# Kernel optimization log

Hardware: AMD Instinct MI355X
Metric: run time of the kernel (lower is better)

Reference implementation:

```python
import jax, jax.numpy as jnp
import numpy as np

HEAD_DIM = 64
WINDOW = 32  # conv_kernel_size


def setup_inputs() -> dict:
    key = jax.random.key(0)
    k0, k1, k2, k3, k4 = jax.random.split(key, 5)
    B, S, H, D = 2, 2048, 8, HEAD_DIM
    return {
        "q": jax.random.normal(k0, (B, S, H * D), dtype=jnp.float32),
        "k": jax.random.normal(k1, (B, S, H * D), dtype=jnp.float32),
        "v": jax.random.normal(k2, (B, S, H * D), dtype=jnp.float32),
        "a": jax.random.normal(k3, (B, S, H), dtype=jnp.float32),
        "b": jax.random.normal(k4, (B, S, H), dtype=jnp.float32),
    }


def reference(q, k, v, a, b):
    B, S, _ = q.shape
    D = HEAD_DIM
    H = k.shape[-1] // D
    W = WINDOW
    scale = 1.0 / (D ** 0.5)

    qh = q.reshape(B, S, H, D)
    kh = k.reshape(B, S, H, D)
    vh = v.reshape(B, S, H, D)

    # window positions j = i - (W-1) + r, r in [0, W); mask j < 0 (torch slices them away)
    idx = jnp.arange(S)[:, None] - (W - 1) + jnp.arange(W)[None, :]  # [S, W]
    valid = (idx >= 0).astype(q.dtype)                               # [S, W]
    idxc = jnp.clip(idx, 0, S - 1)

    k_win = kh[:, idxc]   # [B, S, W, H, D]
    v_win = vh[:, idxc]   # [B, S, W, H, D]
    a_win = a[:, idxc]    # [B, S, W, H]

    scores = jnp.einsum('bshd,bswhd->bswh', qh, k_win) * scale       # [B, S, W, H]
    gates = jax.nn.sigmoid(a_win * b[:, :, None, :])                 # sigmoid(a_j * b_i)
    w = scores * gates * valid[None, :, :, None]

    out = jnp.einsum('bswh,bswhd->bshd', w, v_win)                   # [B, S, H, D]
    return out.reshape(B, S, H * D)
```

## Files before the change

kernel.cpp:

```cpp
#include <hip/hip_runtime.h>
#include <hip/hip_bf16.h>

#define S_LEN 2048
#define H_NUM 8
#define D_DIM 64
#define W_WIN 32

typedef short bf16x8 __attribute__((ext_vector_type(8)));
typedef float f32x4  __attribute__((ext_vector_type(4)));

__device__ __forceinline__ int kswz(int row, int b) {
    return (row << 7) + (b ^ ((row & 7) << 4));
}
__device__ __forceinline__ short f2bf(float x) {
    __hip_bfloat16 h = __float2bfloat16(x);
    return *reinterpret_cast<short*>(&h);
}
__device__ __forceinline__ bf16x8 pack8(float4 a, float4 b) {
    bf16x8 r;
    r[0] = f2bf(a.x); r[1] = f2bf(a.y); r[2] = f2bf(a.z); r[3] = f2bf(a.w);
    r[4] = f2bf(b.x); r[5] = f2bf(b.y); r[6] = f2bf(b.z); r[7] = f2bf(b.w);
    return r;
}
__device__ __forceinline__ int sclamp(int s) {
    return s < 0 ? 0 : (s > S_LEN - 1 ? S_LEN - 1 : s);
}

__global__ __launch_bounds__(64) void swa_gated_direct(
    const float* __restrict__ q, const float* __restrict__ k,
    const float* __restrict__ v, const float* __restrict__ a,
    const float* __restrict__ bgate, float* __restrict__ out)
{
    __shared__ __align__(16) unsigned short w_s[16 * 64];
    char* wb = (char*)w_s;

    const int l  = threadIdx.x;
    const int lr = l & 15;
    const int lk = l >> 4;

    const int bid  = blockIdx.x;
    const int orig = ((bid & 7) << 8) | (bid >> 3);
    const int tile = orig & 127;
    const int h    = (orig >> 7) & 7;
    const int bb   = orig >> 10;
    const int q0   = tile * 16;
    const size_t HD = (size_t)H_NUM * D_DIM;

    const float* qrow = q + ((size_t)(bb * S_LEN + q0 + lr)) * HD + (size_t)h * D_DIM + 8 * lk;
    bf16x8 aq0 = pack8(*(const float4*)(qrow),      *(const float4*)(qrow + 4));
    bf16x8 aq1 = pack8(*(const float4*)(qrow + 32), *(const float4*)(qrow + 36));

    f32x4 c[3];
    #pragma unroll
    for (int n = 0; n < 3; ++n) {
        int kseq = q0 - (W_WIN - 1) + 16 * n + lr;
        const float* krow = k + ((size_t)(bb * S_LEN + sclamp(kseq))) * HD + (size_t)h * D_DIM + 8 * lk;
        bf16x8 b0 = pack8(*(const float4*)(krow),      *(const float4*)(krow + 4));
        bf16x8 b1 = pack8(*(const float4*)(krow + 32), *(const float4*)(krow + 36));
        f32x4 z = {0.f, 0.f, 0.f, 0.f};
        z    = __builtin_amdgcn_mfma_f32_16x16x32_bf16(aq0, b0, z, 0, 0, 0);
        c[n] = __builtin_amdgcn_mfma_f32_16x16x32_bf16(aq1, b1, z, 0, 0, 0);
    }

    const float* vcol = v + ((size_t)bb * S_LEN) * HD + (size_t)h * D_DIM + lr;
    bf16x8 vf0[4], vf1[4];
    #pragma unroll
    for (int n = 0; n < 4; ++n) {
        #pragma unroll
        for (int j = 0; j < 8; ++j) {
            int r0 = q0 - (W_WIN - 1) + 8 * lk + j;
            vf0[n][j] = f2bf(vcol[(size_t)sclamp(r0)      * HD + 16 * n]);
            vf1[n][j] = f2bf(vcol[(size_t)sclamp(r0 + 32) * HD + 16 * n]);
        }
    }

    float bq[4];
    #pragma unroll
    for (int i = 0; i < 4; ++i)
        bq[i] = bgate[((size_t)(bb * S_LEN + q0 + 4 * lk + i)) * H_NUM + h];

    const float scale = 0.125f;
    #pragma unroll
    for (int n = 0; n < 3; ++n) {
        int j    = 16 * n + lr;
        int kseq = q0 - (W_WIN - 1) + j;
        float av = a[((size_t)(bb * S_LEN + sclamp(kseq))) * H_NUM + h];
        #pragma unroll
        for (int i = 0; i < 4; ++i) {
            int qq = 4 * lk + i;
            bool valid = (j >= qq) && (j <= qq + 31) && (kseq >= 0);
            float g  = 1.0f / (1.0f + __expf(-(av * bq[i])));
            float wt = valid ? c[n][i] * scale * g : 0.0f;
            *(unsigned short*)(wb + kswz(qq, j * 2)) = (unsigned short)f2bf(wt);
        }
    }
    *(uint2*)(wb + kswz(lr, 96 + 8 * lk)) = make_uint2(0u, 0u);

    bf16x8 aw0 = *(const bf16x8*)(wb + kswz(lr, 16 * lk));
    bf16x8 aw1 = *(const bf16x8*)(wb + kswz(lr, 16 * lk + 64));

    float* obase = out + ((size_t)(bb * S_LEN + q0)) * HD + (size_t)h * D_DIM;
    #pragma unroll
    for (int n = 0; n < 4; ++n) {
        f32x4 z = {0.f, 0.f, 0.f, 0.f};
        z        = __builtin_amdgcn_mfma_f32_16x16x32_bf16(aw0, vf0[n], z, 0, 0, 0);
        f32x4 o  = __builtin_amdgcn_mfma_f32_16x16x32_bf16(aw1, vf1[n], z, 0, 0, 0);
        #pragma unroll
        for (int i = 0; i < 4; ++i) {
            obase[(size_t)(4 * lk + i) * HD + 16 * n + lr] = o[i];
        }
    }
}

extern "C" void kernel_launch(void* const* d_in, const int* in_sizes, int n_in,
                              void* d_out, int out_size, void* d_ws, size_t ws_size,
                              hipStream_t stream) {
    const float* q  = (const float*)d_in[0];
    const float* k  = (const float*)d_in[1];
    const float* v  = (const float*)d_in[2];
    const float* a  = (const float*)d_in[3];
    const float* bg = (const float*)d_in[4];
    float* out = (float*)d_out;

    dim3 grid(2  * H_NUM * (S_LEN / 16));
    swa_gated_direct<<<grid, 64, 0, stream>>>(q, k, v, a, bg, out);
}
```

Measured before the change: 13.47 us.

## Stage V through LDS with transpose reads and split head dim across waves

Blocks grow to four waves, each handling a 16-query tile and half of the head dimension. V is loaded with coalesced float4 reads, packed to bf16 in LDS, and fed to the MFMA through ds_read_b64_tr_b16 transpose loads, replacing the old strided scalar per-column V gathers. The bf16 packing and the sigmoid reciprocal also use cheaper intrinsics. In exchange, each wave redundantly recomputes the QK scores and gate for its dh half, and correctness now depends on hand-written inline asm and explicit waitcnt.

```diff
diff --git a/kernel.cpp b/kernel.cpp
--- a/kernel.cpp
+++ b/kernel.cpp
@@ -7,6 +7,7 @@
 #define W_WIN 32
 
 typedef short bf16x8 __attribute__((ext_vector_type(8)));
+typedef int   i32x2  __attribute__((ext_vector_type(2)));
 typedef float f32x4  __attribute__((ext_vector_type(4)));
 
 __device__ __forceinline__ int kswz(int row, int b) {
@@ -17,43 +18,66 @@
     return *reinterpret_cast<short*>(&h);
 }
 __device__ __forceinline__ bf16x8 pack8(float4 a, float4 b) {
-    bf16x8 r;
-    r[0] = f2bf(a.x); r[1] = f2bf(a.y); r[2] = f2bf(a.z); r[3] = f2bf(a.w);
-    r[4] = f2bf(b.x); r[5] = f2bf(b.y); r[6] = f2bf(b.z); r[7] = f2bf(b.w);
-    return r;
+    union { __hip_bfloat162 h[4]; bf16x8 v; } u;
+    u.h[0] = __float22bfloat162_rn(make_float2(a.x, a.y));
+    u.h[1] = __float22bfloat162_rn(make_float2(a.z, a.w));
+    u.h[2] = __float22bfloat162_rn(make_float2(b.x, b.y));
+    u.h[3] = __float22bfloat162_rn(make_float2(b.z, b.w));
+    return u.v;
+}
+__device__ __forceinline__ uint2 pack4(float4 a) {
+    union { __hip_bfloat162 h[2]; uint2 v; } u;
+    u.h[0] = __float22bfloat162_rn(make_float2(a.x, a.y));
+    u.h[1] = __float22bfloat162_rn(make_float2(a.z, a.w));
+    return u.v;
 }
 __device__ __forceinline__ int sclamp(int s) {
     return s < 0 ? 0 : (s > S_LEN - 1 ? S_LEN - 1 : s);
 }
 
-__global__ __launch_bounds__(64) void swa_gated_direct(
+__global__ __launch_bounds__(256, 4) void swa_gated_split(
     const float* __restrict__ q, const float* __restrict__ k,
     const float* __restrict__ v, const float* __restrict__ a,
     const float* __restrict__ bgate, float* __restrict__ out)
 {
-    __shared__ __align__(16) unsigned short w_s[16 * 64];
-    char* wb = (char*)w_s;
+    __shared__ __align__(16) unsigned short v_s[4][64 * 32];
+    __shared__ __align__(16) unsigned short w_s[4][16 * 64];
 
-    const int l  = threadIdx.x;
-    const int lr = l & 15;
-    const int lk = l >> 4;
+    const int tid = threadIdx.x;
+    const int wid = tid >> 6;
+    const int l   = tid & 63;
+    const int lr  = l & 15;
+    const int lk  = l >> 4;
+    const int qt  = wid & 1;
+    const int dh  = wid >> 1;
 
     const int bid  = blockIdx.x;
-    const int orig = ((bid & 7) << 8) | (bid >> 3);
-    const int tile = orig & 127;
-    const int h    = (orig >> 7) & 7;
-    const int bb   = orig >> 10;
-    const int q0   = tile * 16;
+    const int orig = ((bid & 7) << 7) | (bid >> 3);
+    const int tile = orig & 63;
+    const int h    = (orig >> 6) & 7;
+    const int bb   = orig >> 9;
+    const int qbase = tile * 32 + 16 * qt;
+    const int wbase = qbase - (W_WIN - 1);
     const size_t HD = (size_t)H_NUM * D_DIM;
 
-    const float* qrow = q + ((size_t)(bb * S_LEN + q0 + lr)) * HD + (size_t)h * D_DIM + 8 * lk;
+    float4 vld[8];
+    #pragma unroll
+    for (int it = 0; it < 8; ++it) {
+        int idx = 64 * it + l;
+        int wr = idx >> 3, c4 = idx & 7;
+        int sc = sclamp(wbase + wr);
+        vld[it] = *(const float4*)(v + ((size_t)(bb * S_LEN + sc)) * HD
+                                     + (size_t)h * D_DIM + 32 * dh + 4 * c4);
+    }
+
+    const float* qrow = q + ((size_t)(bb * S_LEN + qbase + lr)) * HD + (size_t)h * D_DIM + 8 * lk;
     bf16x8 aq0 = pack8(*(const float4*)(qrow),      *(const float4*)(qrow + 4));
     bf16x8 aq1 = pack8(*(const float4*)(qrow + 32), *(const float4*)(qrow + 36));
 
     f32x4 c[3];
     #pragma unroll
     for (int n = 0; n < 3; ++n) {
-        int kseq = q0 - (W_WIN - 1) + 16 * n + lr;
+        int kseq = wbase + 16 * n + lr;
         const float* krow = k + ((size_t)(bb * S_LEN + sclamp(kseq))) * HD + (size_t)h * D_DIM + 8 * lk;
         bf16x8 b0 = pack8(*(const float4*)(krow),      *(const float4*)(krow + 4));
         bf16x8 b1 = pack8(*(const float4*)(krow + 32), *(const float4*)(krow + 36));
@@ -62,52 +86,75 @@
         c[n] = __builtin_amdgcn_mfma_f32_16x16x32_bf16(aq1, b1, z, 0, 0, 0);
     }
 
-    const float* vcol = v + ((size_t)bb * S_LEN) * HD + (size_t)h * D_DIM + lr;
-    bf16x8 vf0[4], vf1[4];
+    unsigned short* Vw = v_s[wid];
     #pragma unroll
-    for (int n = 0; n < 4; ++n) {
-        #pragma unroll
-        for (int j = 0; j < 8; ++j) {
-            int r0 = q0 - (W_WIN - 1) + 8 * lk + j;
-            vf0[n][j] = f2bf(vcol[(size_t)sclamp(r0)      * HD + 16 * n]);
-            vf1[n][j] = f2bf(vcol[(size_t)sclamp(r0 + 32) * HD + 16 * n]);
-        }
+    for (int it = 0; it < 8; ++it) {
+        int idx = 64 * it + l;
+        int wr = idx >> 3, c4 = idx & 7;
+        int db = c4 >> 2, cl = 4 * (c4 & 3);
+        int elem = ((db * 16 + (wr >> 2)) << 6) + ((wr & 3) << 4) + cl;
+        *(uint2*)&Vw[elem] = pack4(vld[it]);
     }
 
+    char* wb = (char*)w_s[wid];
     float bq[4];
     #pragma unroll
     for (int i = 0; i < 4; ++i)
-        bq[i] = bgate[((size_t)(bb * S_LEN + q0 + 4 * lk + i)) * H_NUM + h];
+        bq[i] = bgate[((size_t)(bb * S_LEN + qbase + 4 * lk + i)) * H_NUM + h];
 
     const float scale = 0.125f;
     #pragma unroll
     for (int n = 0; n < 3; ++n) {
         int j    = 16 * n + lr;
-        int kseq = q0 - (W_WIN - 1) + j;
-        float av = a[((size_t)(bb * S_LEN + sclamp(kseq))) * H_NUM + h];
+        int seqk = wbase + j;
+        float av = a[((size_t)(bb * S_LEN + sclamp(seqk))) * H_NUM + h];
         #pragma unroll
         for (int i = 0; i < 4; ++i) {
             int qq = 4 * lk + i;
-            bool valid = (j >= qq) && (j <= qq + 31) && (kseq >= 0);
-            float g  = 1.0f / (1.0f + __expf(-(av * bq[i])));
+            bool valid = (j >= qq) && (j <= qq + 31) && (seqk >= 0);
+            float g  = __builtin_amdgcn_rcpf(1.0f + __expf(-(av * bq[i])));
             float wt = valid ? c[n][i] * scale * g : 0.0f;
-            *(unsigned short*)(wb + kswz(qq, j * 2)) = (unsigned short)f2bf(wt);
+            *(unsigned short*)(wb + kswz(qq, 2 * j)) = (unsigned short)f2bf(wt);
         }
     }
     *(uint2*)(wb + kswz(lr, 96 + 8 * lk)) = make_uint2(0u, 0u);
 
     bf16x8 aw0 = *(const bf16x8*)(wb + kswz(lr, 16 * lk));
-    bf16x8 aw1 = *(const bf16x8*)(wb + kswz(lr, 16 * lk + 64));
+    bf16x8 aw1 = *(const bf16x8*)(wb + kswz(lr, 64 + 16 * lk));
 
-    float* obase = out + ((size_t)(bb * S_LEN + q0)) * HD + (size_t)h * D_DIM;
+    unsigned vbase = (unsigned)(uintptr_t)Vw;
+    asm volatile("s_waitcnt lgkmcnt(0)" ::: "memory");
+    i32x2 t[2][2][2];
     #pragma unroll
-    for (int n = 0; n < 4; ++n) {
-        f32x4 z = {0.f, 0.f, 0.f, 0.f};
-        z        = __builtin_amdgcn_mfma_f32_16x16x32_bf16(aw0, vf0[n], z, 0, 0, 0);
-        f32x4 o  = __builtin_amdgcn_mfma_f32_16x16x32_bf16(aw1, vf1[n], z, 0, 0, 0);
+    for (int kb = 0; kb < 2; ++kb) {
+        #pragma unroll
+        for (int nn = 0; nn < 2; ++nn) {
+            unsigned a0 = vbase + (unsigned)((nn * 16 + 8 * kb + 2 * lk) * 128 + lr * 8);
+            asm volatile("ds_read_b64_tr_b16 %0, %1" : "=v"(t[kb][nn][0]) : "v"(a0));
+            asm volatile("ds_read_b64_tr_b16 %0, %1" : "=v"(t[kb][nn][1]) : "v"(a0 + 128u));
+        }
+    }
+    asm volatile("s_waitcnt lgkmcnt(0)");
+    __builtin_amdgcn_sched_barrier(0);
+
+    f32x4 o[2] = {{0.f,0.f,0.f,0.f},{0.f,0.f,0.f,0.f}};
+    #pragma unroll
+    for (int nn = 0; nn < 2; ++nn) {
+        #pragma unroll
+        for (int kb = 0; kb < 2; ++kb) {
+            union { i32x2 p[2]; bf16x8 v; } bu;
+            bu.p[0] = t[kb][nn][0];
+            bu.p[1] = t[kb][nn][1];
+            o[nn] = __builtin_amdgcn_mfma_f32_16x16x32_bf16(kb ? aw1 : aw0, bu.v, o[nn], 0, 0, 0);
+        }
+    }
+
+    float* obase = out + ((size_t)(bb * S_LEN + qbase)) * HD + (size_t)h * D_DIM + 32 * dh;
+    #pragma unroll
+    for (int nn = 0; nn < 2; ++nn) {
         #pragma unroll
         for (int i = 0; i < 4; ++i) {
-            obase[(size_t)(4 * lk + i) * HD + 16 * n + lr] = o[i];
+            obase[(size_t)(4 * lk + i) * HD + 16 * nn + lr] = o[nn][i];
         }
     }
 }
@@ -122,6 +169,6 @@
     const float* bg = (const float*)d_in[4];
     float* out = (float*)d_out;
 
-    dim3 grid(2  * H_NUM * (S_LEN / 16));
-    swa_gated_direct<<<grid, 64, 0, stream>>>(q, k, v, a, bg, out);
+    dim3 grid(2  * H_NUM * (S_LEN / 32));
+    swa_gated_split<<<grid, 256, 0, stream>>>(q, k, v, a, bg, out);
 }
```

Result: slower. 17.93 us (+33.2%).
